# Kernel tuning notes

Measured on AMD Instinct MI355X. Metric: run time of the kernel, lower is better.

Reference implementation:

```python
import jax, jax.numpy as jnp
import numpy as np

NH, NOPE, ROPE, VD, KVL = 16, 128, 64, 128, 512
QHD = NOPE + ROPE  # 192
EPS = 1e-6
THETA = 10000.0


def rmsnorm(x, w):
    v = jnp.mean(x.astype(jnp.float32) ** 2, axis=-1, keepdims=True)
    return w * (x * jax.lax.rsqrt(v + EPS)).astype(x.dtype)


def _interleave_perm(x):
    # x.view(..., d//2, 2).transpose(-1, -2).reshape(..., d): [x0,x2,...,x1,x3,...]
    return jnp.concatenate([x[..., 0::2], x[..., 1::2]], axis=-1)


def _rotate_half(x):
    d = x.shape[-1] // 2
    return jnp.concatenate([-x[..., d:], x[..., :d]], axis=-1)


def _rope(x, cos, sin):
    x = _interleave_perm(x)
    return x * cos + _rotate_half(x) * sin


def reference(hidden_states, position_ids, q_a_w, q_a_ln, q_b_w, kv_a_w, kv_a_ln, kv_b_w, o_w):
    B, S, _ = hidden_states.shape
    h = hidden_states

    # low-rank Q: q_b(rmsnorm(q_a(h)))
    q = rmsnorm(h @ q_a_w.T, q_a_ln) @ q_b_w.T          # [B,S,NH*192]
    q = q.reshape(B, S, NH, QHD).transpose(0, 2, 1, 3)   # [B,NH,S,192]
    q_nope, q_pe = q[..., :NOPE], q[..., NOPE:]

    # compressed KV + shared rope key
    ckv = h @ kv_a_w.T                                    # [B,S,KVL+ROPE]
    compressed, k_pe = ckv[..., :KVL], ckv[..., KVL:]
    k_pe = k_pe.reshape(B, S, 1, ROPE).transpose(0, 2, 1, 3)  # [B,1,S,ROPE]

    kv = rmsnorm(compressed, kv_a_ln) @ kv_b_w.T          # [B,S,NH*(NOPE+VD)]
    kv = kv.reshape(B, S, NH, NOPE + VD).transpose(0, 2, 1, 3)
    k_nope, v = kv[..., :NOPE], kv[..., NOPE:]            # [B,NH,S,*]

    # rotary cache
    inv_freq = 1.0 / (THETA ** (jnp.arange(0, ROPE, 2, dtype=jnp.float32) / ROPE))
    t = jnp.arange(S, dtype=jnp.float32)
    freqs = jnp.outer(t, inv_freq)
    emb = jnp.concatenate([freqs, freqs], axis=-1)        # [S,ROPE]
    cos = jnp.cos(emb)[position_ids][:, None]             # [B,1,S,ROPE]
    sin = jnp.sin(emb)[position_ids][:, None]

    q_pe = _rope(q_pe, cos, sin)
    k_pe = _rope(k_pe, cos, sin)

    query = jnp.concatenate([q_nope, q_pe], axis=-1)                       # [B,NH,S,192]
    key = jnp.concatenate([k_nope, jnp.broadcast_to(k_pe, (B, NH, S, ROPE))], axis=-1)

    scale = QHD ** -0.5
    scores = jnp.einsum('bhqd,bhkd->bhqk', query, key) * scale
    causal = jnp.tril(jnp.ones((S, S), dtype=bool))
    scores = jnp.where(causal, scores, jnp.finfo(scores.dtype).min)
    attn = jax.nn.softmax(scores.astype(jnp.float32), axis=-1).astype(query.dtype)

    out = jnp.einsum('bhqk,bhkd->bhqd', attn, v)          # [B,NH,S,VD]
    out = out.transpose(0, 2, 1, 3).reshape(B, S, NH * VD)
    return out @ o_w.T


def setup_inputs():
    key = jax.random.key(0)
    ks = jax.random.split(key, 7)
    B, S, HID, QL = 2, 1024, 2048, 1536
    w = lambda i, shape: jax.random.normal(ks[i], shape, jnp.float32) / np.sqrt(shape[-1])
    return {
        'hidden_states': jax.random.normal(ks[0], (B, S, HID), jnp.float32),
        'position_ids': jnp.tile(jnp.arange(S, dtype=jnp.int32)[None, :], (B, 1)),
        'q_a_w': w(1, (QL, HID)),
        'q_a_ln': jnp.ones((QL,), jnp.float32),
        'q_b_w': w(2, (NH * QHD, QL)),
        'kv_a_w': w(3, (KVL + ROPE, HID)),
        'kv_a_ln': jnp.ones((KVL,), jnp.float32),
        'kv_b_w': w(4, (NH * (NOPE + VD), KVL)),
        'o_w': w(5, (HID, NH * VD)),
    }
```

## Files before the change

### kernel.cpp

```cpp
#include <hip/hip_runtime.h>
#include <stdint.h>
#include <math.h>

typedef unsigned short u16;
typedef __attribute__((ext_vector_type(8))) short short8;
typedef __attribute__((ext_vector_type(4))) short short4v;
typedef __attribute__((ext_vector_type(4))) float f32x4;

#define DEVFN static __device__ __forceinline__

DEVFN float bf2f(short b) {
  union { unsigned int i; float f; } u;
  u.i = ((unsigned int)(unsigned short)b) << 16;
  return u.f;
}
DEVFN short f2bf(float f) {
  union { float f; unsigned int i; } u; u.f = f;
  unsigned int r = u.i + 0x7fffu + ((u.i >> 16) & 1u);
  return (short)(r >> 16);
}

DEVFN f32x4 mfma32(short8 a, short8 b, f32x4 c) {
  return __builtin_amdgcn_mfma_f32_16x16x32_bf16(a, b, c, 0, 0, 0);
}
DEVFN f32x4 mfma16(short4v a, short4v b, f32x4 c) {
#if defined(__HIP_DEVICE_COMPILE__)
  return __builtin_amdgcn_mfma_f32_16x16x16bf16_1k(a, b, c, 0, 0, 0);
#else
  (void)a; (void)b; return c;
#endif
}

typedef const __attribute__((address_space(1))) unsigned int* gp_t;
typedef __attribute__((address_space(3))) unsigned int* lp_t;
typedef const __attribute__((address_space(3))) u16* lds_cp;
DEVFN void async_copy16(u16* lds, const u16* g) {
  __builtin_amdgcn_global_load_lds((gp_t)(const void*)g, (lp_t)(void*)lds, 16, 0, 0);
}
DEVFN short4v tr_read16(const u16* p) {
  short4v r;
  asm volatile("ds_read_b64_tr_b16 %0, %1" : "=v"(r) : "v"((lds_cp)(const void*)p));
  return r;
}
DEVFN void raw_barrier() {
  asm volatile("" ::: "memory");
  __builtin_amdgcn_s_barrier();
  asm volatile("" ::: "memory");
}

__global__ void cast_kernel(const float* __restrict__ in, u16* __restrict__ out, int n4) {
  int i = blockIdx.x * blockDim.x + threadIdx.x;
  if (i < n4) {
    f32x4 v = ((const f32x4*)in)[i];
    short4v o;
    o[0] = f2bf(v[0]); o[1] = f2bf(v[1]); o[2] = f2bf(v[2]); o[3] = f2bf(v[3]);
    ((short4v*)out)[i] = o;
  }
}

__global__ void rmsnorm_kernel(const u16* __restrict__ in, int istride,
                               u16* __restrict__ out, int ostride,
                               const float* __restrict__ w, int len) {
  const int row = blockIdx.x, t = threadIdx.x;
  short8 v = *(const short8*)(in + (size_t)row * istride + t * 8);
  float f[8]; float ss = 0.f;
#pragma unroll
  for (int j = 0; j < 8; ++j) { f[j] = bf2f(v[j]); ss += f[j] * f[j]; }
#pragma unroll
  for (int off = 1; off < 64; off <<= 1) ss += __shfl_xor(ss, off);
  __shared__ float red[8];
  int nw = (int)blockDim.x >> 6;
  if ((t & 63) == 0) red[t >> 6] = ss;
  __syncthreads();
  ss = 0.f;
  for (int i = 0; i < nw; ++i) ss += red[i];
  float r = rsqrtf(ss / (float)len + 1e-6f);
  const float* wp = w + t * 8;
  short8 ov;
#pragma unroll
  for (int j = 0; j < 8; ++j) ov[j] = f2bf(f[j] * r * wp[j]);
  *(short8*)(out + (size_t)row * ostride + t * 8) = ov;
}

__global__ void rope_kernel(const u16* __restrict__ q, const u16* __restrict__ ckv,
                            const int* __restrict__ pos_ids,
                            u16* __restrict__ qpe, u16* __restrict__ kpe) {
  const int row = blockIdx.x;
  const int t = threadIdx.x;
  const float pos = (float)pos_ids[row];
  const float L2TH = 13.287712379549449f;
  if (t < 32) {
    int i = t;
    float inv = exp2f(-L2TH * (float)i / 32.0f);
    float sv, cv; sincosf(pos * inv, &sv, &cv);
    float x0 = bf2f(ckv[(size_t)row * 576 + 512 + 2 * i]);
    float x1 = bf2f(ckv[(size_t)row * 576 + 512 + 2 * i + 1]);
    kpe[(size_t)row * 64 + i]      = (u16)f2bf(x0 * cv - x1 * sv);
    kpe[(size_t)row * 64 + 32 + i] = (u16)f2bf(x1 * cv + x0 * sv);
  }
#pragma unroll
  for (int j = 0; j < 8; ++j) {
    int idx = t + 64 * j;
    int hh = idx >> 5, i = idx & 31;
    float inv = exp2f(-L2TH * (float)i / 32.0f);
    float sv, cv; sincosf(pos * inv, &sv, &cv);
    const u16* base = q + (size_t)row * 3072 + hh * 192 + 128;
    float x0 = bf2f(base[2 * i]), x1 = bf2f(base[2 * i + 1]);
    u16* ob = qpe + ((size_t)row * 16 + hh) * 64;
    ob[i]      = (u16)f2bf(x0 * cv - x1 * sv);
    ob[32 + i] = (u16)f2bf(x1 * cv + x0 * sv);
  }
}

template <int BM, bool OUT_F32, int TAG>
__global__ __launch_bounds__(256) void gemm_bt(const u16* __restrict__ A,
                                               const u16* __restrict__ B,
                                               void* __restrict__ C,
                                               int M, int N, int K, int ldc) {
  constexpr int ACH = BM / 32;
  constexpr int MI  = BM / 32;
  __shared__ u16 As[2][BM * 64];
  __shared__ u16 Bs[2][64 * 64];
  const int tid = threadIdx.x;
  const int w = tid >> 6, l = tid & 63;
  const int lq = l & 15, lg = l >> 4;
  const int wm = (w >> 1) * (BM / 2);
  const int wn = (w & 1) << 5;
  const int m0 = blockIdx.y * BM, n0 = blockIdx.x << 6;

  const u16* srcA[ACH]; int dstA[ACH];
#pragma unroll
  for (int i = 0; i < ACH; ++i) {
    int c = i * 256 + tid;
    int row = c >> 3, pc = c & 7;
    int lc = pc ^ (row & 7);
    srcA[i] = A + (size_t)(m0 + row) * K + lc * 8;
    dstA[i] = c * 8;
  }
  const u16* srcB[2]; int dstB[2];
#pragma unroll
  for (int i = 0; i < 2; ++i) {
    int c = i * 256 + tid;
    int row = c >> 3, pc = c & 7;
    int lc = pc ^ (row & 7);
    srcB[i] = B + (size_t)(n0 + row) * K + lc * 8;
    dstB[i] = c * 8;
  }

  auto stage = [&](int buf) {
#pragma unroll
    for (int i = 0; i < ACH; ++i) {
      async_copy16(&As[buf][dstA[i]], srcA[i]);
      srcA[i] += 64;
    }
#pragma unroll
    for (int i = 0; i < 2; ++i) {
      async_copy16(&Bs[buf][dstB[i]], srcB[i]);
      srcB[i] += 64;
    }
  };

  f32x4 acc[MI][2];
#pragma unroll
  for (int i = 0; i < MI; ++i)
#pragma unroll
    for (int j = 0; j < 2; ++j) acc[i][j] = (f32x4){0.f, 0.f, 0.f, 0.f};

  const int nt = K >> 6;
  stage(0);
  if (nt > 1) stage(1);

  for (int t = 0; t < nt; ++t) {
    if (t + 1 < nt) {
      if constexpr (BM == 128)
        asm volatile("s_waitcnt vmcnt(6)" ::: "memory");
      else
        asm volatile("s_waitcnt vmcnt(4)" ::: "memory");
    } else {
      asm volatile("s_waitcnt vmcnt(0)" ::: "memory");
    }
    raw_barrier();

    const int buf = t & 1;
#pragma unroll
    for (int ks = 0; ks < 2; ++ks) {
      short8 af[MI], bfr[2];
#pragma unroll
      for (int mi = 0; mi < MI; ++mi) {
        int row = wm + mi * 16 + lq;
        int ch = ((ks << 2) | lg) ^ (row & 7);
        af[mi] = *(const short8*)&As[buf][row * 64 + ch * 8];
      }
#pragma unroll
      for (int ni = 0; ni < 2; ++ni) {
        int row = wn + ni * 16 + lq;
        int ch = ((ks << 2) | lg) ^ (row & 7);
        bfr[ni] = *(const short8*)&Bs[buf][row * 64 + ch * 8];
      }
#pragma unroll
      for (int mi = 0; mi < MI; ++mi)
#pragma unroll
        for (int ni = 0; ni < 2; ++ni)
          acc[mi][ni] = mfma32(af[mi], bfr[ni], acc[mi][ni]);
    }

    raw_barrier();
    if (t + 2 < nt) stage(buf);
  }

#pragma unroll
  for (int mi = 0; mi < MI; ++mi) {
#pragma unroll
    for (int ni = 0; ni < 2; ++ni) {
      int col = n0 + wn + ni * 16 + lq;
#pragma unroll
      for (int r = 0; r < 4; ++r) {
        int rowm = m0 + wm + mi * 16 + lg * 4 + r;
        if constexpr (OUT_F32)
          ((float*)C)[(size_t)rowm * ldc + col] = acc[mi][ni][r];
        else
          ((u16*)C)[(size_t)rowm * ldc + col] = (u16)f2bf(acc[mi][ni][r]);
      }
    }
  }
}

__global__ __launch_bounds__(256) void attn_kernel(const u16* __restrict__ q,
                                                   const u16* __restrict__ qpe,
                                                   const u16* __restrict__ kv,
                                                   const u16* __restrict__ kpe,
                                                   u16* __restrict__ o) {
  __shared__ u16 Ks[2][64 * 192];
  __shared__ u16 Vs[2][64 * 128];
  const int S = 1024;
  const int tid = threadIdx.x;
  const int w = tid >> 6, l = tid & 63;
  const int lq = l & 15, lg = l >> 4;
  const int h = blockIdx.y, b = blockIdx.z;
  const int chunk = b ? (15 - (int)blockIdx.x) : (int)blockIdx.x;
  const int q0 = chunk * 64 + w * 16;
  const int nkt = chunk + 1;
  const size_t qrow = (size_t)b * S + q0 + lq;

  short8 qf[6];
#pragma unroll
  for (int c = 0; c < 4; ++c)
    qf[c] = *(const short8*)(q + qrow * 3072 + h * 192 + c * 32 + lg * 8);
#pragma unroll
  for (int c = 0; c < 2; ++c)
    qf[4 + c] = *(const short8*)(qpe + (qrow * 16 + h) * 64 + c * 32 + lg * 8);

  const size_t gb = (size_t)b * S;
  const u16* srcK[6]; int strK[6];
#pragma unroll
  for (int j = 0; j < 6; ++j) {
    int n = w * 384 + j * 64 + l;
    int row = (n * 2731) >> 16;
    int pc = n - row * 24;
    int lc = (pc & ~7) | ((pc & 7) ^ (row & 7));
    if (lc < 16) { srcK[j] = kv + (gb + row) * 4096 + h * 256 + lc * 8; strK[j] = 64 * 4096; }
    else         { srcK[j] = kpe + (gb + row) * 64 + (lc - 16) * 8;     strK[j] = 64 * 64; }
  }
  const u16* srcV[4];
#pragma unroll
  for (int j = 0; j < 4; ++j) {
    int n = w * 256 + j * 64 + l;
    int s = n >> 3, hh = n & 7;
    int dsub = s >> 4, ksub = s & 15;
    int krow = hh >> 1, dhalf = hh & 1;
    srcV[j] = kv + (gb + ksub * 4 + krow) * 4096 + h * 256 + 128 + dsub * 16 + dhalf * 8;
  }

  auto stage = [&](int buf) {
#pragma unroll
    for (int j = 0; j < 6; ++j) {
      async_copy16(&Ks[buf][(w * 384 + j * 64) * 8], srcK[j]);
      srcK[j] += strK[j];
    }
#pragma unroll
    for (int j = 0; j < 4; ++j) {
      async_copy16(&Vs[buf][(w * 256 + j * 64) * 8], srcV[j]);
      srcV[j] += 64 * 4096;
    }
  };

  const float scl = 0.07216878364870323f * 1.4426950408889634f;
  float m2 = -INFINITY, lsum = 0.f;
  f32x4 oac[8];
#pragma unroll
  for (int dt = 0; dt < 8; ++dt) oac[dt] = (f32x4){0.f, 0.f, 0.f, 0.f};

  const int e0 = (lg ^ (lq & 7)) << 4;
  const int vbase = lg * 64 + lq * 4;

  stage(0);
  asm volatile("s_waitcnt vmcnt(0)" ::: "memory");
  __syncthreads();

  int buf = 0;
  for (int kt = 0; kt < nkt; ++kt) {
    if (kt + 1 < nkt) stage(buf ^ 1);

    const char* kb = (const char*)&Ks[buf][0];
    f32x4 sac[4];
#pragma unroll
    for (int kt2 = 0; kt2 < 4; ++kt2) {
      int a0 = (kt2 * 16 + lq) * 384 + e0;
      int a1 = a0 ^ 64;
      f32x4 s = (f32x4){0.f, 0.f, 0.f, 0.f};
      s = mfma32(*(const short8*)(kb + a0),       qf[0], s);
      s = mfma32(*(const short8*)(kb + a1),       qf[1], s);
      s = mfma32(*(const short8*)(kb + a0 + 128), qf[2], s);
      s = mfma32(*(const short8*)(kb + a1 + 128), qf[3], s);
      s = mfma32(*(const short8*)(kb + a0 + 256), qf[4], s);
      s = mfma32(*(const short8*)(kb + a1 + 256), qf[5], s);
      sac[kt2] = s;
    }

    short4v vf[8][4];
#pragma unroll
    for (int dt = 0; dt < 8; ++dt)
#pragma unroll
      for (int kt2 = 0; kt2 < 4; ++kt2)
        vf[dt][kt2] = tr_read16(&Vs[buf][vbase + dt * 1024 + kt2 * 256]);

    const int qi = q0 + lq;
    const int kb0 = kt * 64 + lg * 4;
    float s2[16];
#pragma unroll
    for (int kt2 = 0; kt2 < 4; ++kt2)
#pragma unroll
      for (int r = 0; r < 4; ++r)
        s2[kt2 * 4 + r] = (kb0 + kt2 * 16 + r <= qi) ? sac[kt2][r] * scl : -INFINITY;
    float mt = s2[0];
#pragma unroll
    for (int r = 1; r < 16; ++r) mt = fmaxf(mt, s2[r]);
    mt = fmaxf(mt, __shfl_xor(mt, 16));
    mt = fmaxf(mt, __shfl_xor(mt, 32));
    float mnew = fmaxf(m2, mt);
    float resc = exp2f(m2 - mnew);
    float p[16], psum = 0.f;
#pragma unroll
    for (int r = 0; r < 16; ++r) { p[r] = exp2f(s2[r] - mnew); psum += p[r]; }
    psum += __shfl_xor(psum, 16);
    psum += __shfl_xor(psum, 32);
    lsum = lsum * resc + psum;
    m2 = mnew;
    short4v pf[4];
#pragma unroll
    for (int kt2 = 0; kt2 < 4; ++kt2)
#pragma unroll
      for (int r = 0; r < 4; ++r) pf[kt2][r] = f2bf(p[kt2 * 4 + r]);

    asm volatile("s_waitcnt lgkmcnt(0)" ::: "memory");
    __builtin_amdgcn_sched_barrier(0);
#pragma unroll
    for (int dt = 0; dt < 8; ++dt) {
      f32x4 t = oac[dt];
      t[0] *= resc; t[1] *= resc; t[2] *= resc; t[3] *= resc;
#pragma unroll
      for (int kt2 = 0; kt2 < 4; ++kt2) t = mfma16(vf[dt][kt2], pf[kt2], t);
      oac[dt] = t;
    }

    asm volatile("s_waitcnt vmcnt(0)" ::: "memory");
    __syncthreads();
    buf ^= 1;
  }

  float inv = 1.f / lsum;
#pragma unroll
  for (int dt = 0; dt < 8; ++dt)
#pragma unroll
    for (int r = 0; r < 4; ++r)
      o[((size_t)b * S + q0 + lq) * 2048 + h * 128 + dt * 16 + lg * 4 + r] =
          (u16)f2bf(oac[dt][r] * inv);
}

extern "C" void kernel_launch(void* const* d_in, const int* in_sizes, int n_in,
                              void* d_out, int out_size, void* d_ws, size_t ws_size,
                              hipStream_t stream) {
  const float* h_in  = (const float*)d_in[0];
  const int*   pos   = (const int*)d_in[1];
  const float* qaw   = (const float*)d_in[2];
  const float* qaln  = (const float*)d_in[3];
  const float* qbw   = (const float*)d_in[4];
  const float* kvaw  = (const float*)d_in[5];
  const float* kvaln = (const float*)d_in[6];
  const float* kvbw  = (const float*)d_in[7];
  const float* ow    = (const float*)d_in[8];
  float* out = (float*)d_out;

  const int M = 2048;
  char* p = (char*)d_ws;
  auto alloc = [&](size_t bytes) {
    char* r = p;
    p += (bytes + 255) & ~(size_t)255;
    return (u16*)r;
  };
  u16* h_bf = alloc((size_t)M * 2048 * 2);
  u16* W    = alloc((size_t)3072 * 1536 * 2);
  u16* qa   = alloc((size_t)M * 1536 * 2);
  u16* qbuf = alloc((size_t)M * 3072 * 2);
  u16* kvb  = alloc((size_t)M * 4096 * 2);
  u16* qpe  = alloc((size_t)M * 16 * 64 * 2);
  u16* kpe  = alloc((size_t)M * 64 * 2);
  u16* ckv  = qa;
  u16* ckvn = qa + (size_t)M * 576;
  u16* attno = h_bf;

  dim3 blk(256);

  cast_kernel<<<4096, blk, 0, stream>>>(h_in, h_bf, 1048576);
  cast_kernel<<<3072, blk, 0, stream>>>(qaw, W, 786432);
  gemm_bt<128, false, 1><<<dim3(24, 16), blk, 0, stream>>>(h_bf, W, qa, M, 1536, 2048, 1536);
  rmsnorm_kernel<<<2048, 192, 0, stream>>>(qa, 1536, qa, 1536, qaln, 1536);

  cast_kernel<<<4608, blk, 0, stream>>>(qbw, W, 1179648);
  gemm_bt<128, false, 2><<<dim3(48, 16), blk, 0, stream>>>(qa, W, qbuf, M, 3072, 1536, 3072);

  cast_kernel<<<1152, blk, 0, stream>>>(kvaw, W, 294912);
  gemm_bt<64, false, 3><<<dim3(9, 32), blk, 0, stream>>>(h_bf, W, ckv, M, 576, 2048, 576);
  rmsnorm_kernel<<<2048, 64, 0, stream>>>(ckv, 576, ckvn, 512, kvaln, 512);

  cast_kernel<<<2048, blk, 0, stream>>>(kvbw, W, 524288);
  gemm_bt<128, false, 4><<<dim3(64, 16), blk, 0, stream>>>(ckvn, W, kvb, M, 4096, 512, 4096);

  rope_kernel<<<2048, 64, 0, stream>>>(qbuf, ckv, pos, qpe, kpe);

  attn_kernel<<<dim3(16, 16, 2), blk, 0, stream>>>(qbuf, qpe, kvb, kpe, attno);

  cast_kernel<<<4096, blk, 0, stream>>>(ow, W, 1048576);
  gemm_bt<128, true, 5><<<dim3(32, 16), blk, 0, stream>>>(attno, W, out, M, 2048, 2048, 2048);
}
```

Before: 206.4 us.

## Split attention KV tiles across two wave teams and swizzle GEMM block order

The attention kernel now runs 512 threads per block as two teams of four waves. Each team processes alternating 32-key halves of every 64-key tile, and waves skip half-tiles that the causal mask hides entirely. The two teams' partial softmax states are merged through shared memory at the end. This doubles the waves available to hide latency, at the cost of an extra reduction step, a block-wide barrier and register pressure under the launch_bounds(512,4) hint. Separately, the GEMM remaps block indices with an 8-way interleave, likely to spread neighbouring output tiles across XCDs or improve cache locality.

```diff
diff --git a/kernel.cpp b/kernel.cpp
--- a/kernel.cpp
+++ b/kernel.cpp
@@ -126,7 +126,12 @@
   const int lq = l & 15, lg = l >> 4;
   const int wm = (w >> 1) * (BM / 2);
   const int wn = (w & 1) << 5;
-  const int m0 = blockIdx.y * BM, n0 = blockIdx.x << 6;
+
+  const int f = blockIdx.x + gridDim.x * blockIdx.y;
+  const int nwg = gridDim.x * gridDim.y;
+  const int swz = (f & 7) * (nwg >> 3) + (f >> 3);
+  const int bx = swz % gridDim.x, by = swz / gridDim.x;
+  const int m0 = by * BM, n0 = bx << 6;
 
   const u16* srcA[ACH]; int dstA[ACH];
 #pragma unroll
@@ -225,20 +230,21 @@
   }
 }
 
-__global__ __launch_bounds__(256) void attn_kernel(const u16* __restrict__ q,
-                                                   const u16* __restrict__ qpe,
-                                                   const u16* __restrict__ kv,
-                                                   const u16* __restrict__ kpe,
-                                                   u16* __restrict__ o) {
-  __shared__ u16 Ks[2][64 * 192];
-  __shared__ u16 Vs[2][64 * 128];
+__global__ __launch_bounds__(512, 4) void attn_kernel(const u16* __restrict__ q,
+                                                      const u16* __restrict__ qpe,
+                                                      const u16* __restrict__ kv,
+                                                      const u16* __restrict__ kpe,
+                                                      u16* __restrict__ o) {
+  __shared__ u16 Ks[2][2][32 * 192];
+  __shared__ u16 Vs[2][2][32 * 128];
   const int S = 1024;
   const int tid = threadIdx.x;
   const int w = tid >> 6, l = tid & 63;
+  const int team = w >> 2, wt = w & 3;
   const int lq = l & 15, lg = l >> 4;
   const int h = blockIdx.y, b = blockIdx.z;
   const int chunk = b ? (15 - (int)blockIdx.x) : (int)blockIdx.x;
-  const int q0 = chunk * 64 + w * 16;
+  const int q0 = chunk * 64 + wt * 16;
   const int nkt = chunk + 1;
   const size_t qrow = (size_t)b * S + q0 + lq;
 
@@ -250,36 +256,35 @@
   for (int c = 0; c < 2; ++c)
     qf[4 + c] = *(const short8*)(qpe + (qrow * 16 + h) * 64 + c * 32 + lg * 8);
 
-  const size_t gb = (size_t)b * S;
-  const u16* srcK[6]; int strK[6];
-#pragma unroll
-  for (int j = 0; j < 6; ++j) {
-    int n = w * 384 + j * 64 + l;
+  const size_t gb = (size_t)b * S + 32 * team;
+  const u16* srcK[3]; int strK[3];
+#pragma unroll
+  for (int j = 0; j < 3; ++j) {
+    int n = wt * 192 + j * 64 + l;
     int row = (n * 2731) >> 16;
     int pc = n - row * 24;
     int lc = (pc & ~7) | ((pc & 7) ^ (row & 7));
     if (lc < 16) { srcK[j] = kv + (gb + row) * 4096 + h * 256 + lc * 8; strK[j] = 64 * 4096; }
     else         { srcK[j] = kpe + (gb + row) * 64 + (lc - 16) * 8;     strK[j] = 64 * 64; }
   }
-  const u16* srcV[4];
-#pragma unroll
-  for (int j = 0; j < 4; ++j) {
-    int n = w * 256 + j * 64 + l;
-    int s = n >> 3, hh = n & 7;
-    int dsub = s >> 4, ksub = s & 15;
-    int krow = hh >> 1, dhalf = hh & 1;
-    srcV[j] = kv + (gb + ksub * 4 + krow) * 4096 + h * 256 + 128 + dsub * 16 + dhalf * 8;
+  const u16* srcV[2];
+#pragma unroll
+  for (int j = 0; j < 2; ++j) {
+    int n = wt * 128 + j * 64 + l;
+    int dsub = n >> 6, m = n & 63;
+    int ksub = m >> 3, r = (m >> 1) & 3, half = m & 1;
+    srcV[j] = kv + (gb + ksub * 4 + r) * 4096 + h * 256 + 128 + dsub * 16 + half * 8;
   }
 
   auto stage = [&](int buf) {
 #pragma unroll
-    for (int j = 0; j < 6; ++j) {
-      async_copy16(&Ks[buf][(w * 384 + j * 64) * 8], srcK[j]);
+    for (int j = 0; j < 3; ++j) {
+      async_copy16(&Ks[buf][team][(wt * 192 + j * 64) * 8], srcK[j]);
       srcK[j] += strK[j];
     }
 #pragma unroll
-    for (int j = 0; j < 4; ++j) {
-      async_copy16(&Vs[buf][(w * 256 + j * 64) * 8], srcV[j]);
+    for (int j = 0; j < 2; ++j) {
+      async_copy16(&Vs[buf][team][(wt * 128 + j * 64) * 8], srcV[j]);
       srcV[j] += 64 * 4096;
     }
   };
@@ -298,69 +303,69 @@
   __syncthreads();
 
   int buf = 0;
-  for (int kt = 0; kt < nkt; ++kt) {
-    if (kt + 1 < nkt) stage(buf ^ 1);
-
-    const char* kb = (const char*)&Ks[buf][0];
-    f32x4 sac[4];
-#pragma unroll
-    for (int kt2 = 0; kt2 < 4; ++kt2) {
-      int a0 = (kt2 * 16 + lq) * 384 + e0;
-      int a1 = a0 ^ 64;
-      f32x4 s = (f32x4){0.f, 0.f, 0.f, 0.f};
-      s = mfma32(*(const short8*)(kb + a0),       qf[0], s);
-      s = mfma32(*(const short8*)(kb + a1),       qf[1], s);
-      s = mfma32(*(const short8*)(kb + a0 + 128), qf[2], s);
-      s = mfma32(*(const short8*)(kb + a1 + 128), qf[3], s);
-      s = mfma32(*(const short8*)(kb + a0 + 256), qf[4], s);
-      s = mfma32(*(const short8*)(kb + a1 + 256), qf[5], s);
-      sac[kt2] = s;
-    }
-
-    short4v vf[8][4];
-#pragma unroll
-    for (int dt = 0; dt < 8; ++dt)
-#pragma unroll
-      for (int kt2 = 0; kt2 < 4; ++kt2)
-        vf[dt][kt2] = tr_read16(&Vs[buf][vbase + dt * 1024 + kt2 * 256]);
-
-    const int qi = q0 + lq;
-    const int kb0 = kt * 64 + lg * 4;
-    float s2[16];
-#pragma unroll
-    for (int kt2 = 0; kt2 < 4; ++kt2)
-#pragma unroll
-      for (int r = 0; r < 4; ++r)
-        s2[kt2 * 4 + r] = (kb0 + kt2 * 16 + r <= qi) ? sac[kt2][r] * scl : -INFINITY;
-    float mt = s2[0];
-#pragma unroll
-    for (int r = 1; r < 16; ++r) mt = fmaxf(mt, s2[r]);
-    mt = fmaxf(mt, __shfl_xor(mt, 16));
-    mt = fmaxf(mt, __shfl_xor(mt, 32));
-    float mnew = fmaxf(m2, mt);
-    float resc = exp2f(m2 - mnew);
-    float p[16], psum = 0.f;
-#pragma unroll
-    for (int r = 0; r < 16; ++r) { p[r] = exp2f(s2[r] - mnew); psum += p[r]; }
-    psum += __shfl_xor(psum, 16);
-    psum += __shfl_xor(psum, 32);
-    lsum = lsum * resc + psum;
-    m2 = mnew;
-    short4v pf[4];
-#pragma unroll
-    for (int kt2 = 0; kt2 < 4; ++kt2)
-#pragma unroll
-      for (int r = 0; r < 4; ++r) pf[kt2][r] = f2bf(p[kt2 * 4 + r]);
-
-    asm volatile("s_waitcnt lgkmcnt(0)" ::: "memory");
-    __builtin_amdgcn_sched_barrier(0);
-#pragma unroll
-    for (int dt = 0; dt < 8; ++dt) {
-      f32x4 t = oac[dt];
-      t[0] *= resc; t[1] *= resc; t[2] *= resc; t[3] *= resc;
-#pragma unroll
-      for (int kt2 = 0; kt2 < 4; ++kt2) t = mfma16(vf[dt][kt2], pf[kt2], t);
-      oac[dt] = t;
+  for (int i = 0; i < nkt; ++i) {
+    if (i + 1 < nkt) stage(buf ^ 1);
+    const int kbase = (2 * i + team) * 32;
+
+    if (kbase <= q0 + 15) {
+      const char* kb = (const char*)&Ks[buf][team][0];
+      f32x4 sac0, sac1;
+#pragma unroll
+      for (int kt2 = 0; kt2 < 2; ++kt2) {
+        int a0 = (kt2 * 16 + lq) * 384 + e0;
+        int a1 = a0 ^ 64;
+        f32x4 s = (f32x4){0.f, 0.f, 0.f, 0.f};
+        s = mfma32(*(const short8*)(kb + a0),       qf[0], s);
+        s = mfma32(*(const short8*)(kb + a1),       qf[1], s);
+        s = mfma32(*(const short8*)(kb + a0 + 128), qf[2], s);
+        s = mfma32(*(const short8*)(kb + a1 + 128), qf[3], s);
+        s = mfma32(*(const short8*)(kb + a0 + 256), qf[4], s);
+        s = mfma32(*(const short8*)(kb + a1 + 256), qf[5], s);
+        if (kt2 == 0) sac0 = s; else sac1 = s;
+      }
+
+      short4v vf[8][2];
+#pragma unroll
+      for (int dt = 0; dt < 8; ++dt)
+#pragma unroll
+        for (int kt2 = 0; kt2 < 2; ++kt2)
+          vf[dt][kt2] = tr_read16(&Vs[buf][team][vbase + dt * 512 + kt2 * 256]);
+
+      const int qi = q0 + lq;
+      const int kb0 = kbase + lg * 4;
+      float s2[8];
+#pragma unroll
+      for (int r = 0; r < 4; ++r) {
+        s2[r]     = (kb0 + r      <= qi) ? sac0[r] * scl : -INFINITY;
+        s2[4 + r] = (kb0 + 16 + r <= qi) ? sac1[r] * scl : -INFINITY;
+      }
+      float mt = fmaxf(fmaxf(fmaxf(s2[0], s2[1]), fmaxf(s2[2], s2[3])),
+                       fmaxf(fmaxf(s2[4], s2[5]), fmaxf(s2[6], s2[7])));
+      mt = fmaxf(mt, __shfl_xor(mt, 16));
+      mt = fmaxf(mt, __shfl_xor(mt, 32));
+      float mnew = fmaxf(m2, mt);
+      float resc = exp2f(m2 - mnew);
+      float pp[8], psum = 0.f;
+#pragma unroll
+      for (int r = 0; r < 8; ++r) { pp[r] = exp2f(s2[r] - mnew); psum += pp[r]; }
+      psum += __shfl_xor(psum, 16);
+      psum += __shfl_xor(psum, 32);
+      lsum = lsum * resc + psum;
+      m2 = mnew;
+      short4v pf0, pf1;
+#pragma unroll
+      for (int r = 0; r < 4; ++r) { pf0[r] = f2bf(pp[r]); pf1[r] = f2bf(pp[4 + r]); }
+
+      asm volatile("s_waitcnt lgkmcnt(0)" ::: "memory");
+      __builtin_amdgcn_sched_barrier(0);
+#pragma unroll
+      for (int dt = 0; dt < 8; ++dt) {
+        f32x4 t = oac[dt];
+        t[0] *= resc; t[1] *= resc; t[2] *= resc; t[3] *= resc;
+        t = mfma16(vf[dt][0], pf0, t);
+        t = mfma16(vf[dt][1], pf1, t);
+        oac[dt] = t;
+      }
     }
 
     asm volatile("s_waitcnt vmcnt(0)" ::: "memory");
@@ -368,13 +373,31 @@
     buf ^= 1;
   }
 
-  float inv = 1.f / lsum;
-#pragma unroll
-  for (int dt = 0; dt < 8; ++dt)
-#pragma unroll
-    for (int r = 0; r < 4; ++r)
-      o[((size_t)b * S + q0 + lq) * 2048 + h * 128 + dt * 16 + lg * 4 + r] =
-          (u16)f2bf(oac[dt][r] * inv);
+  float* MO = (float*)&Ks[0][0][0];
+  float* MS = (float*)&Vs[0][0][0];
+  const int qr = wt * 16 + lq;
+  if (team == 1) {
+#pragma unroll
+    for (int dt = 0; dt < 8; ++dt)
+#pragma unroll
+      for (int r = 0; r < 4; ++r)
+        MO[qr * 129 + dt * 16 + lg * 4 + r] = oac[dt][r];
+    if (lg == 0) { MS[qr * 2] = m2; MS[qr * 2 + 1] = lsum; }
+  }
+  __syncthreads();
+  if (team == 0) {
+    float m1 = MS[qr * 2], l1 = MS[qr * 2 + 1];
+    float mn = fmaxf(m2, m1);
+    float a0 = exp2f(m2 - mn), a1 = exp2f(m1 - mn);
+    float inv = 1.f / (lsum * a0 + l1 * a1);
+#pragma unroll
+    for (int dt = 0; dt < 8; ++dt)
+#pragma unroll
+      for (int r = 0; r < 4; ++r) {
+        float val = (oac[dt][r] * a0 + MO[qr * 129 + dt * 16 + lg * 4 + r] * a1) * inv;
+        o[((size_t)b * S + q0 + lq) * 2048 + h * 128 + dt * 16 + lg * 4 + r] = (u16)f2bf(val);
+      }
+  }
 }
 
 extern "C" void kernel_launch(void* const* d_in, const int* in_sizes, int n_in,
@@ -428,7 +451,7 @@
 
   rope_kernel<<<2048, 64, 0, stream>>>(qbuf, ckv, pos, qpe, kpe);
 
-  attn_kernel<<<dim3(16, 16, 2), blk, 0, stream>>>(qbuf, qpe, kvb, kpe, attno);
+  attn_kernel<<<dim3(16, 16, 2), 512, 0, stream>>>(qbuf, qpe, kvb, kpe, attno);
 
   cast_kernel<<<4096, blk, 0, stream>>>(ow, W, 1048576);
   gemm_bt<128, true, 5><<<dim3(32, 16), blk, 0, stream>>>(attno, W, out, M, 2048, 2048, 2048);
```

New measurement: 236.8 us. 14.7% more time.
